# Kernel tuning notes

Measured on AMD Instinct MI355X. Metric: run time of the kernel, lower is better.

Reference implementation:

```python
import jax, jax.numpy as jnp
import numpy as np

N_USER = 50000
N_ITEM = 50000
N_EDGE = 1600000
D_IN = 64
D_OUT = 64


def _mean_agg(msgs, dst, num_dst):
    # copy_u + mean: segment-mean of edge messages onto dst nodes; zero for
    # zero-in-degree nodes (DGL default).
    s = jax.ops.segment_sum(msgs, dst, num_segments=num_dst)          # [Nd, D]
    cnt = jax.ops.segment_sum(jnp.ones((msgs.shape[0],), msgs.dtype), dst,
                              num_segments=num_dst)                    # [Nd]
    return s / jnp.maximum(cnt, 1.0)[:, None]


def setup_inputs() -> dict:
    key = jax.random.key(0)
    ks = jax.random.split(key, 12)
    return {
        'user_feat': jax.random.normal(ks[0], (N_USER, D_IN), jnp.float32),
        'item_feat': jax.random.normal(ks[1], (N_ITEM, D_IN), jnp.float32),
        'rate_src': jax.random.randint(ks[2], (N_EDGE,), 0, N_USER, jnp.int64 if jax.config.jax_enable_x64 else jnp.int32),
        'rate_dst': jax.random.randint(ks[3], (N_EDGE,), 0, N_ITEM, jnp.int64 if jax.config.jax_enable_x64 else jnp.int32),
        'rev_src': jax.random.randint(ks[4], (N_EDGE,), 0, N_ITEM, jnp.int64 if jax.config.jax_enable_x64 else jnp.int32),
        'rev_dst': jax.random.randint(ks[5], (N_EDGE,), 0, N_USER, jnp.int64 if jax.config.jax_enable_x64 else jnp.int32),
        'W_rate': jax.random.normal(ks[6], (D_IN, D_OUT), jnp.float32) * (1.0 / np.sqrt(D_IN)),
        'b_rate': jnp.zeros((D_OUT,), jnp.float32),
        'W_rev': jax.random.normal(ks[7], (D_IN, D_OUT), jnp.float32) * (1.0 / np.sqrt(D_IN)),
        'b_rev': jnp.zeros((D_OUT,), jnp.float32),
        'loop_weight': jax.random.normal(ks[8], (D_IN, D_OUT), jnp.float32) * (1.0 / np.sqrt(D_IN)),
        'h_bias': jnp.zeros((D_OUT,), jnp.float32),
    }


def reference(user_feat, item_feat, rate_src, rate_dst, rev_src, rev_dst,
              W_rate, b_rate, W_rev, b_rev, loop_weight, h_bias):
    # Per-etype Linear on source-node features (applied node-wise, as in torch).
    Wh_rate = user_feat @ W_rate + b_rate      # [Nu, Dout], etype 'rate': user->item
    Wh_rev = item_feat @ W_rev + b_rev         # [Ni, Dout], etype 'rated-by': item->user

    # copy_u + mean per etype, cross-reduce 'sum' (one etype per dst ntype here).
    h_item = _mean_agg(Wh_rate[rate_src], rate_dst, N_ITEM)
    h_user = _mean_agg(Wh_rev[rev_src], rev_dst, N_USER)

    # self-loop + bias (dropout p=0.0 is identity)
    h_user = h_user + user_feat @ loop_weight + h_bias
    h_item = h_item + item_feat @ loop_weight + h_bias
    return (h_user, h_item)
```

## Files before the change

kernel.cpp:

```cpp
#include <hip/hip_runtime.h>

#define N_USER 50000
#define N_ITEM 50000
#define N_NODE 50000
#define N_EDGE 1600000
#define D 64

#define FB_SHIFT 7
#define N_FINE 400
#define CAP 5120
#define CHUNK 8192

typedef __attribute__((ext_vector_type(8))) short short8;
typedef __attribute__((ext_vector_type(4))) float floatx4;

__device__ __forceinline__ unsigned short f32_to_bf16(float x) {
    unsigned u = __float_as_uint(x);
    unsigned r = (u + 0x7FFFu + ((u >> 16) & 1u)) >> 16;
    return (unsigned short)r;
}
__device__ __forceinline__ float bf16_to_f32(unsigned short h) {
    return __uint_as_float(((unsigned)h) << 16);
}

__global__ __launch_bounds__(256) void cast_kernel(
    const float4* __restrict__ inU, ushort4* __restrict__ outU,
    const float4* __restrict__ inI, ushort4* __restrict__ outI, int n4)
{
    const float4* __restrict__ in = blockIdx.y ? inI : inU;
    ushort4* __restrict__ out     = blockIdx.y ? outI : outU;
    int i = blockIdx.x * 256 + threadIdx.x;
    if (i < n4) {
        float4 v = in[i];
        ushort4 o;
        o.x = f32_to_bf16(v.x); o.y = f32_to_bf16(v.y);
        o.z = f32_to_bf16(v.z); o.w = f32_to_bf16(v.w);
        out[i] = o;
    }
}

__global__ __launch_bounds__(1024) void init_fcur(int* __restrict__ fcur)
{
    int i = threadIdx.x;
    if (i < 2 * N_FINE) {
        int f = (i < N_FINE) ? i : i - N_FINE;
        fcur[i] = f * CAP;
    }
}

__global__ __launch_bounds__(256) void fine_bin(
    const int* __restrict__ srcA, const int* __restrict__ dstA, unsigned* __restrict__ binA,
    const int* __restrict__ srcB, const int* __restrict__ dstB, unsigned* __restrict__ binB,
    int* __restrict__ fcur)
{
    const int et = blockIdx.y;
    const int* __restrict__ src = et ? srcB : srcA;
    const int* __restrict__ dst = et ? dstB : dstA;
    unsigned* __restrict__ bin  = et ? binB : binA;
    int* __restrict__ fc = fcur + et * N_FINE;

    __shared__ int hist[N_FINE];
    __shared__ int lcur[N_FINE];
    for (int i = threadIdx.x; i < N_FINE; i += 256) hist[i] = 0;
    __syncthreads();

    const int base = blockIdx.x * CHUNK;
    const int n4 = (min(CHUNK, N_EDGE - base)) >> 2;
    const int4* dst4 = (const int4*)(dst + base);
    const int4* src4 = (const int4*)(src + base);

    for (int i = threadIdx.x; i < n4; i += 256) {
        int4 d = dst4[i];
        atomicAdd(&hist[d.x >> FB_SHIFT], 1);
        atomicAdd(&hist[d.y >> FB_SHIFT], 1);
        atomicAdd(&hist[d.z >> FB_SHIFT], 1);
        atomicAdd(&hist[d.w >> FB_SHIFT], 1);
    }
    __syncthreads();
    for (int f = threadIdx.x; f < N_FINE; f += 256) {
        int c = hist[f];
        lcur[f] = c ? atomicAdd(&fc[f], c) : 0;
    }
    __syncthreads();
    for (int i = threadIdx.x; i < n4; i += 256) {
        int4 d = dst4[i];
        int4 s = src4[i];
        { int pos = atomicAdd(&lcur[d.x >> FB_SHIFT], 1); bin[pos] = ((unsigned)d.x << 16) | (unsigned)s.x; }
        { int pos = atomicAdd(&lcur[d.y >> FB_SHIFT], 1); bin[pos] = ((unsigned)d.y << 16) | (unsigned)s.y; }
        { int pos = atomicAdd(&lcur[d.z >> FB_SHIFT], 1); bin[pos] = ((unsigned)d.z << 16) | (unsigned)s.z; }
        { int pos = atomicAdd(&lcur[d.w >> FB_SHIFT], 1); bin[pos] = ((unsigned)d.w << 16) | (unsigned)s.w; }
    }
}

__global__ __launch_bounds__(256) void bucket_sort(
    const unsigned* __restrict__ binI, unsigned short* __restrict__ srtI,
    int* __restrict__ offI, int* __restrict__ cntI,
    const unsigned* __restrict__ binU, unsigned short* __restrict__ srtU,
    int* __restrict__ offU, int* __restrict__ cntU,
    const int* __restrict__ fcur)
{
    const int et = blockIdx.y;
    const unsigned* __restrict__ bin = et ? binU : binI;
    unsigned short* __restrict__ srt = et ? srtU : srtI;
    int* __restrict__ off  = et ? offU : offI;
    int* __restrict__ cntG = et ? cntU : cntI;
    const int f = blockIdx.x;
    const int start = f * CAP;
    const int end   = fcur[et * N_FINE + f];
    const int nodebase = f << FB_SHIFT;

    __shared__ int cnt[128];
    __shared__ int sc[128];
    __shared__ int pos[128];
    if (threadIdx.x < 128) cnt[threadIdx.x] = 0;
    __syncthreads();

    for (int e = start + threadIdx.x; e < end; e += 256) {
        int ld = (int)(bin[e] >> 16) - nodebase;
        atomicAdd(&cnt[ld], 1);
    }
    __syncthreads();

    if (threadIdx.x < 128) sc[threadIdx.x] = cnt[threadIdx.x];
    __syncthreads();
    for (int o = 1; o < 128; o <<= 1) {
        int t = 0;
        if (threadIdx.x < 128 && threadIdx.x >= o) t = sc[threadIdx.x - o];
        __syncthreads();
        if (threadIdx.x < 128) sc[threadIdx.x] += t;
        __syncthreads();
    }
    if (threadIdx.x < 128) {
        int base = start + sc[threadIdx.x] - cnt[threadIdx.x];
        pos[threadIdx.x] = base;
        int node = nodebase + threadIdx.x;
        if (node < N_NODE) { off[node] = base; cntG[node] = cnt[threadIdx.x]; }
    }
    __syncthreads();

    for (int e = start + threadIdx.x; e < end; e += 256) {
        unsigned p = bin[e];
        int ld = (int)(p >> 16) - nodebase;
        int q = atomicAdd(&pos[ld], 1);
        srt[q] = (unsigned short)(p & 0xFFFFu);
    }
}

__global__ __launch_bounds__(256) void aggregate_kernel(
    const ushort4* __restrict__ itemB,
    const ushort4* __restrict__ userB,
    const int* __restrict__ offU, const int* __restrict__ cntU, const unsigned short* __restrict__ srtU,
    const int* __restrict__ offI, const int* __restrict__ cntI, const unsigned short* __restrict__ srtI,
    ushort4* __restrict__ aggU, ushort4* __restrict__ aggI)
{
    int g = blockIdx.x * 16 + (threadIdx.x >> 4);
    if (g >= N_USER + N_ITEM) return;
    const int lane = threadIdx.x & 15;

    const bool isUser = (g < N_USER);
    const int d = isUser ? g : g - N_USER;
    const ushort4* __restrict__ tab = isUser ? itemB : userB;
    const int* __restrict__ off     = isUser ? offU : offI;
    const int* __restrict__ cntG    = isUser ? cntU : cntI;
    const unsigned short* __restrict__ srt = isUser ? srtU : srtI;
    ushort4* __restrict__ agg       = isUser ? aggU : aggI;

    const int start = off[d];
    const int c     = cntG[d];
    const int end   = start + c;

    float4 a0 = make_float4(0.f, 0.f, 0.f, 0.f);
    float4 a1 = make_float4(0.f, 0.f, 0.f, 0.f);
    int e = start;
    for (; e + 2 <= end; e += 2) {
        int s0 = (int)srt[e], s1 = (int)srt[e + 1];
        ushort4 w0 = tab[(size_t)s0 * 16 + lane];
        ushort4 w1 = tab[(size_t)s1 * 16 + lane];
        a0.x += bf16_to_f32(w0.x); a0.y += bf16_to_f32(w0.y);
        a0.z += bf16_to_f32(w0.z); a0.w += bf16_to_f32(w0.w);
        a1.x += bf16_to_f32(w1.x); a1.y += bf16_to_f32(w1.y);
        a1.z += bf16_to_f32(w1.z); a1.w += bf16_to_f32(w1.w);
    }
    if (e < end) {
        int s0 = (int)srt[e];
        ushort4 w0 = tab[(size_t)s0 * 16 + lane];
        a0.x += bf16_to_f32(w0.x); a0.y += bf16_to_f32(w0.y);
        a0.z += bf16_to_f32(w0.z); a0.w += bf16_to_f32(w0.w);
    }
    a0.x += a1.x; a0.y += a1.y; a0.z += a1.z; a0.w += a1.w;

    const float inv = (c > 0) ? 1.0f / (float)c : 0.0f;
    ushort4 o;
    o.x = f32_to_bf16(a0.x * inv);
    o.y = f32_to_bf16(a0.y * inv);
    o.z = f32_to_bf16(a0.z * inv);
    o.w = f32_to_bf16(a0.w * inv);
    agg[(size_t)g * 16 + lane - (isUser ? 0 : (size_t)N_USER * 16)] = o;
}

__global__ __launch_bounds__(256, 4) void final_gemm(
    const unsigned short* __restrict__ aggU_, const unsigned short* __restrict__ featU_,
    const int* __restrict__ cntU_, const float* __restrict__ WU,
    const float* __restrict__ beU,
    const unsigned short* __restrict__ aggI_, const unsigned short* __restrict__ featI_,
    const int* __restrict__ cntI_, const float* __restrict__ WI,
    const float* __restrict__ beI,
    const float* __restrict__ loop_w, const float* __restrict__ h_bias,
    float* __restrict__ out)
{
    const int et = blockIdx.y;
    const unsigned short* __restrict__ agg  = et ? aggI_ : aggU_;
    const unsigned short* __restrict__ feat = et ? featI_ : featU_;
    const int* __restrict__ cntG            = et ? cntI_ : cntU_;
    const float* __restrict__ W             = et ? WI : WU;
    const float* __restrict__ b_et          = et ? beI : beU;
    float* __restrict__ outN = out + (et ? (size_t)N_USER * D : 0);

    __shared__ unsigned short sWt[64][72];
    __shared__ unsigned short sLt[64][72];
    __shared__ float sbe[64], sbh[64];
    __shared__ int sCnt[64];

    const int tid = threadIdx.x;
    const int row0 = blockIdx.x * 64;

    for (int i = tid; i < 4096; i += 256) {
        int k = i >> 6, n = i & 63;
        sWt[n][k] = f32_to_bf16(W[i]);
        sLt[n][k] = f32_to_bf16(loop_w[i]);
    }
    if (tid < 64) {
        sbe[tid] = b_et[tid];
        sbh[tid] = h_bias[tid];
        int r = row0 + tid;
        sCnt[tid] = (r < N_NODE) ? cntG[r] : 0;
    }
    __syncthreads();

    const int wave = tid >> 6;
    const int lane = tid & 63;
    const int quad = lane >> 4;
    const int l16  = lane & 15;

    const int rowA = row0 + wave * 16 + l16;
    const int rA = (rowA < N_NODE) ? rowA : (N_NODE - 1);
    short8 aAgg0  = *(const short8*)(agg  + (size_t)rA * 64 +      quad * 8);
    short8 aAgg1  = *(const short8*)(agg  + (size_t)rA * 64 + 32 + quad * 8);
    short8 aFeat0 = *(const short8*)(feat + (size_t)rA * 64 +      quad * 8);
    short8 aFeat1 = *(const short8*)(feat + (size_t)rA * 64 + 32 + quad * 8);

    floatx4 acc[4];
    #pragma unroll
    for (int t = 0; t < 4; ++t) {
        const int n = t * 16 + l16;
        short8 bW0 = *(const short8*)&sWt[n][     quad * 8];
        short8 bW1 = *(const short8*)&sWt[n][32 + quad * 8];
        short8 bL0 = *(const short8*)&sLt[n][     quad * 8];
        short8 bL1 = *(const short8*)&sLt[n][32 + quad * 8];
        floatx4 a = {0.f, 0.f, 0.f, 0.f};
        a = __builtin_amdgcn_mfma_f32_16x16x32_bf16(aAgg0,  bW0, a, 0, 0, 0);
        a = __builtin_amdgcn_mfma_f32_16x16x32_bf16(aAgg1,  bW1, a, 0, 0, 0);
        a = __builtin_amdgcn_mfma_f32_16x16x32_bf16(aFeat0, bL0, a, 0, 0, 0);
        a = __builtin_amdgcn_mfma_f32_16x16x32_bf16(aFeat1, bL1, a, 0, 0, 0);
        acc[t] = a;
    }

    #pragma unroll
    for (int t = 0; t < 4; ++t) {
        const int col = t * 16 + l16;
        const float bh = sbh[col], be = sbe[col];
        #pragma unroll
        for (int i = 0; i < 4; ++i) {
            int lrow = wave * 16 + quad * 4 + i;
            int r = row0 + lrow;
            if (r < N_NODE) {
                float v = acc[t][i] + bh + (sCnt[lrow] > 0 ? be : 0.f);
                outN[(size_t)r * D + col] = v;
            }
        }
    }
}

extern "C" void kernel_launch(void* const* d_in, const int* in_sizes, int n_in,
                              void* d_out, int out_size, void* d_ws, size_t ws_size,
                              hipStream_t stream)
{
    const float* user_feat = (const float*)d_in[0];
    const float* item_feat = (const float*)d_in[1];
    const int*   rate_src  = (const int*)d_in[2];
    const int*   rate_dst  = (const int*)d_in[3];
    const int*   rev_src   = (const int*)d_in[4];
    const int*   rev_dst   = (const int*)d_in[5];
    const float* W_rate    = (const float*)d_in[6];
    const float* b_rate    = (const float*)d_in[7];
    const float* W_rev     = (const float*)d_in[8];
    const float* b_rev     = (const float*)d_in[9];
    const float* loop_w    = (const float*)d_in[10];
    const float* h_bias    = (const float*)d_in[11];
    float* out = (float*)d_out;

    char* p = (char*)d_ws;
    ushort4* userB = (ushort4*)p; p += (size_t)N_USER * D * 2;
    ushort4* itemB = (ushort4*)p; p += (size_t)N_ITEM * D * 2;
    unsigned* binI = (unsigned*)p; p += (size_t)N_FINE * CAP * 4;
    unsigned* binU = (unsigned*)p; p += (size_t)N_FINE * CAP * 4;
    unsigned short* srtI = (unsigned short*)p; p += (size_t)N_FINE * CAP * 2;
    unsigned short* srtU = (unsigned short*)p; p += (size_t)N_FINE * CAP * 2;
    ushort4* aggI  = (ushort4*)p; p += (size_t)N_NODE * D * 2;
    ushort4* aggU  = (ushort4*)p; p += (size_t)N_NODE * D * 2;
    int* offI = (int*)p; p += (size_t)N_NODE * 4;
    int* offU = (int*)p; p += (size_t)N_NODE * 4;
    int* cntI = (int*)p; p += (size_t)N_NODE * 4;
    int* cntU = (int*)p; p += (size_t)N_NODE * 4;
    int* fcur = (int*)p; p += (size_t)(2 * N_FINE) * 4;
    (void)ws_size;

    cast_kernel<<<dim3(3125, 2), 256, 0, stream>>>(
        (const float4*)user_feat, userB, (const float4*)item_feat, itemB, N_NODE * 16);
    init_fcur<<<1, 1024, 0, stream>>>(fcur);

    fine_bin<<<dim3((N_EDGE + CHUNK - 1) / CHUNK, 2), 256, 0, stream>>>(
        rate_src, rate_dst, binI,
        rev_src,  rev_dst,  binU, fcur);

    bucket_sort<<<dim3(N_FINE, 2), 256, 0, stream>>>(
        binI, srtI, offI, cntI,
        binU, srtU, offU, cntU, fcur);

    aggregate_kernel<<<(N_USER + N_ITEM + 15) / 16, 256, 0, stream>>>(
        itemB, userB,
        offU, cntU, srtU,
        offI, cntI, srtI,
        aggU, aggI);

    final_gemm<<<dim3((N_NODE + 63) / 64, 2), 256, 0, stream>>>(
        (const unsigned short*)aggU, (const unsigned short*)userB, cntU, W_rev, b_rev,
        (const unsigned short*)aggI, (const unsigned short*)itemB, cntI, W_rate, b_rate,
        loop_w, h_bias, out);

    (void)in_sizes; (void)n_in; (void)out_size;
}
```

Measured before the change: 240.2 us.

## Fuse feature cast with edge binning and unroll aggregation loop by four

Merges the bf16 cast kernel and the fine-binning kernel into one launch, with blocks split by index between the two jobs. The init_fcur kernel is replaced by a memset, so the bin cursors now hold relative counts and the base offset is added at use. The binning chunk is halved to give more blocks, and the aggregation loop is unrolled to four independent gathers per iteration to raise memory-level parallelism. This cuts launch overhead and lets the cast overlap with binning, at the cost of more global atomics on the cursors and extra register pressure.

```diff
diff --git a/kernel.cpp b/kernel.cpp
--- a/kernel.cpp
+++ b/kernel.cpp
@@ -9,7 +9,9 @@
 #define FB_SHIFT 7
 #define N_FINE 400
 #define CAP 5120
-#define CHUNK 8192
+#define BIN_CHUNK 4096
+#define NCAST 3125
+#define NBIN ((N_EDGE + BIN_CHUNK - 1) / BIN_CHUNK)
 
 typedef __attribute__((ext_vector_type(8))) short short8;
 typedef __attribute__((ext_vector_type(4))) float floatx4;
@@ -23,49 +25,40 @@
     return __uint_as_float(((unsigned)h) << 16);
 }
 
-__global__ __launch_bounds__(256) void cast_kernel(
-    const float4* __restrict__ inU, ushort4* __restrict__ outU,
-    const float4* __restrict__ inI, ushort4* __restrict__ outI, int n4)
-{
-    const float4* __restrict__ in = blockIdx.y ? inI : inU;
-    ushort4* __restrict__ out     = blockIdx.y ? outI : outU;
-    int i = blockIdx.x * 256 + threadIdx.x;
-    if (i < n4) {
+__global__ __launch_bounds__(256) void cast_bin(
+    const float4* __restrict__ fU, ushort4* __restrict__ bU,
+    const float4* __restrict__ fI, ushort4* __restrict__ bI,
+    const int* __restrict__ srcA, const int* __restrict__ dstA, unsigned* __restrict__ binA,
+    const int* __restrict__ srcB, const int* __restrict__ dstB, unsigned* __restrict__ binB,
+    int* __restrict__ fcur)
+{
+    __shared__ int hist[N_FINE];
+    __shared__ int lcur[N_FINE];
+    const int et = blockIdx.y;
+
+    if (blockIdx.x < NCAST) {
+        const float4* __restrict__ in = et ? fI : fU;
+        ushort4* __restrict__ out     = et ? bI : bU;
+        int i = blockIdx.x * 256 + threadIdx.x;
         float4 v = in[i];
         ushort4 o;
         o.x = f32_to_bf16(v.x); o.y = f32_to_bf16(v.y);
         o.z = f32_to_bf16(v.z); o.w = f32_to_bf16(v.w);
         out[i] = o;
-    }
-}
-
-__global__ __launch_bounds__(1024) void init_fcur(int* __restrict__ fcur)
-{
-    int i = threadIdx.x;
-    if (i < 2 * N_FINE) {
-        int f = (i < N_FINE) ? i : i - N_FINE;
-        fcur[i] = f * CAP;
-    }
-}
-
-__global__ __launch_bounds__(256) void fine_bin(
-    const int* __restrict__ srcA, const int* __restrict__ dstA, unsigned* __restrict__ binA,
-    const int* __restrict__ srcB, const int* __restrict__ dstB, unsigned* __restrict__ binB,
-    int* __restrict__ fcur)
-{
-    const int et = blockIdx.y;
+        return;
+    }
+
     const int* __restrict__ src = et ? srcB : srcA;
     const int* __restrict__ dst = et ? dstB : dstA;
     unsigned* __restrict__ bin  = et ? binB : binA;
     int* __restrict__ fc = fcur + et * N_FINE;
 
-    __shared__ int hist[N_FINE];
-    __shared__ int lcur[N_FINE];
     for (int i = threadIdx.x; i < N_FINE; i += 256) hist[i] = 0;
     __syncthreads();
 
-    const int base = blockIdx.x * CHUNK;
-    const int n4 = (min(CHUNK, N_EDGE - base)) >> 2;
+    const int chunk = blockIdx.x - NCAST;
+    const int base = chunk * BIN_CHUNK;
+    const int n4 = (min(BIN_CHUNK, N_EDGE - base)) >> 2;
     const int4* dst4 = (const int4*)(dst + base);
     const int4* src4 = (const int4*)(src + base);
 
@@ -79,7 +72,7 @@
     __syncthreads();
     for (int f = threadIdx.x; f < N_FINE; f += 256) {
         int c = hist[f];
-        lcur[f] = c ? atomicAdd(&fc[f], c) : 0;
+        lcur[f] = c ? (f * CAP + atomicAdd(&fc[f], c)) : 0;
     }
     __syncthreads();
     for (int i = threadIdx.x; i < n4; i += 256) {
@@ -106,7 +99,7 @@
     int* __restrict__ cntG = et ? cntU : cntI;
     const int f = blockIdx.x;
     const int start = f * CAP;
-    const int end   = fcur[et * N_FINE + f];
+    const int end   = start + fcur[et * N_FINE + f];
     const int nodebase = f << FB_SHIFT;
 
     __shared__ int cnt[128];
@@ -171,23 +164,35 @@
 
     float4 a0 = make_float4(0.f, 0.f, 0.f, 0.f);
     float4 a1 = make_float4(0.f, 0.f, 0.f, 0.f);
+    float4 a2 = make_float4(0.f, 0.f, 0.f, 0.f);
+    float4 a3 = make_float4(0.f, 0.f, 0.f, 0.f);
     int e = start;
-    for (; e + 2 <= end; e += 2) {
-        int s0 = (int)srt[e], s1 = (int)srt[e + 1];
+    for (; e + 4 <= end; e += 4) {
+        int s0 = (int)srt[e],     s1 = (int)srt[e + 1];
+        int s2 = (int)srt[e + 2], s3 = (int)srt[e + 3];
         ushort4 w0 = tab[(size_t)s0 * 16 + lane];
         ushort4 w1 = tab[(size_t)s1 * 16 + lane];
+        ushort4 w2 = tab[(size_t)s2 * 16 + lane];
+        ushort4 w3 = tab[(size_t)s3 * 16 + lane];
         a0.x += bf16_to_f32(w0.x); a0.y += bf16_to_f32(w0.y);
         a0.z += bf16_to_f32(w0.z); a0.w += bf16_to_f32(w0.w);
         a1.x += bf16_to_f32(w1.x); a1.y += bf16_to_f32(w1.y);
         a1.z += bf16_to_f32(w1.z); a1.w += bf16_to_f32(w1.w);
-    }
-    if (e < end) {
+        a2.x += bf16_to_f32(w2.x); a2.y += bf16_to_f32(w2.y);
+        a2.z += bf16_to_f32(w2.z); a2.w += bf16_to_f32(w2.w);
+        a3.x += bf16_to_f32(w3.x); a3.y += bf16_to_f32(w3.y);
+        a3.z += bf16_to_f32(w3.z); a3.w += bf16_to_f32(w3.w);
+    }
+    for (; e < end; ++e) {
         int s0 = (int)srt[e];
         ushort4 w0 = tab[(size_t)s0 * 16 + lane];
         a0.x += bf16_to_f32(w0.x); a0.y += bf16_to_f32(w0.y);
         a0.z += bf16_to_f32(w0.z); a0.w += bf16_to_f32(w0.w);
     }
-    a0.x += a1.x; a0.y += a1.y; a0.z += a1.z; a0.w += a1.w;
+    a0.x += a1.x + a2.x + a3.x;
+    a0.y += a1.y + a2.y + a3.y;
+    a0.z += a1.z + a2.z + a3.z;
+    a0.w += a1.w + a2.w + a3.w;
 
     const float inv = (c > 0) ? 1.0f / (float)c : 0.0f;
     ushort4 o;
@@ -315,11 +320,10 @@
     int* fcur = (int*)p; p += (size_t)(2 * N_FINE) * 4;
     (void)ws_size;
 
-    cast_kernel<<<dim3(3125, 2), 256, 0, stream>>>(
-        (const float4*)user_feat, userB, (const float4*)item_feat, itemB, N_NODE * 16);
-    init_fcur<<<1, 1024, 0, stream>>>(fcur);
-
-    fine_bin<<<dim3((N_EDGE + CHUNK - 1) / CHUNK, 2), 256, 0, stream>>>(
+    hipMemsetAsync(fcur, 0, (size_t)(2 * N_FINE) * sizeof(int), stream);
+
+    cast_bin<<<dim3(NCAST + NBIN, 2), 256, 0, stream>>>(
+        (const float4*)user_feat, userB, (const float4*)item_feat, itemB,
         rate_src, rate_dst, binI,
         rev_src,  rev_dst,  binU, fcur);
 
```

New measurement: 235.8 us. Within noise of the previous version (-1.8%).
